# Performance work log

Hardware: AMD Instinct MI355X
Metric: run time of the kernel (lower is better)

## Reference

```python
import jax, jax.numpy as jnp
import numpy as np

N_NODES = 50000
N_EDGES = 800000
D_IN = 128
D_OUT = 128


def setup_inputs() -> dict:
    key = jax.random.key(0)
    k1, k2, k3, k4, k5, k6 = jax.random.split(key, 6)
    x = jax.random.normal(k1, (N_NODES, D_IN), dtype=jnp.float32)
    weight = jax.random.normal(k2, (D_IN, D_OUT), dtype=jnp.float32)
    bias = jax.random.normal(k3, (D_OUT,), dtype=jnp.float32)
    adj_row = jax.random.randint(k4, (N_EDGES,), 0, N_NODES, dtype=jnp.int64)
    adj_col = jax.random.randint(k5, (N_EDGES,), 0, N_NODES, dtype=jnp.int64)
    adj_val = jax.random.uniform(k6, (N_EDGES,), dtype=jnp.float32)
    return {"x": x, "weight": weight, "bias": bias,
            "adj_row": adj_row, "adj_col": adj_col, "adj_val": adj_val}


def reference(x, weight, bias, adj_row, adj_col, adj_val):
    # support = x @ W  -- dense GEMM [N, D_in] x [D_in, D_out]
    support = jnp.matmul(x, weight)
    # spmm(adj, support): out[i] = sum_e adj_val[e] * support[adj_col[e]] for adj_row[e]==i
    messages = support[adj_col] * adj_val[:, None]          # [E, D_out]
    output = jax.ops.segment_sum(messages, adj_row, num_segments=x.shape[0])
    return output + bias
```

## Files before the change

kernel.cpp:

```cpp
#include <hip/hip_runtime.h>

#define D 128
#define ELL_CAP 64
#define EPT 8

typedef __attribute__((ext_vector_type(8))) short short8;
typedef __attribute__((ext_vector_type(4))) float floatx4;
typedef unsigned int uint;
typedef unsigned short ushort;

__device__ inline short f2bf(float f) {
  unsigned u = __float_as_uint(f);
  u += 0x7FFF + ((u >> 16) & 1);
  return (short)(u >> 16);
}

__global__ __launch_bounds__(256) void gemm_scatter_kernel(
    const float* __restrict__ x, const float* __restrict__ w,
    ushort* __restrict__ support, int n_nodes, int gemm_blocks,
    const int* __restrict__ adj_row, const int* __restrict__ adj_col,
    const float* __restrict__ adj_val, int* __restrict__ cnt,
    uint* __restrict__ ell, int n_edges, int range_size) {
  __shared__ short sWA[2 * 8 * 64 * 8];
  const int tid = threadIdx.x;

  if ((int)blockIdx.x < gemm_blocks) {
    const int wid = tid >> 6;
    const int lane = tid & 63;
    const int quad = lane >> 4;
    const int node = blockIdx.x * 64 + wid * 16 + (lane & 15);
    const bool ok = (node < n_nodes);

    floatx4 acc[8];
#pragma unroll
    for (int mt = 0; mt < 8; ++mt) acc[mt] = (floatx4){0.f, 0.f, 0.f, 0.f};

#pragma unroll
    for (int kt2 = 0; kt2 < 4; kt2 += 2) {
      if (kt2) __syncthreads();
      for (int s = tid; s < 1024; s += 256) {
        int ktmt = s >> 6, ls = s & 63;
        int kt = kt2 + (ktmt >> 3);
        int kb = kt * 32 + (ls >> 4) * 8;
        int m = (ktmt & 7) * 16 + (ls & 15);
        short8 frag;
#pragma unroll
        for (int j = 0; j < 8; ++j) frag[j] = f2bf(w[(kb + j) * D + m]);
        *(short8*)&sWA[s * 8] = frag;
      }
      __syncthreads();

#pragma unroll
      for (int ktoff = 0; ktoff < 2; ++ktoff) {
        const int kt = kt2 + ktoff;
        short8 bfr = (short8){0, 0, 0, 0, 0, 0, 0, 0};
        if (ok) {
          const float4 v0 = *(const float4*)&x[(size_t)node * D + kt * 32 + quad * 8];
          const float4 v1 = *(const float4*)&x[(size_t)node * D + kt * 32 + quad * 8 + 4];
          bfr = (short8){f2bf(v0.x), f2bf(v0.y), f2bf(v0.z), f2bf(v0.w),
                         f2bf(v1.x), f2bf(v1.y), f2bf(v1.z), f2bf(v1.w)};
        }
#pragma unroll
        for (int mt = 0; mt < 8; ++mt) {
          short8 a = *(const short8*)&sWA[((ktoff * 8 + mt) * 64 + lane) * 8];
          acc[mt] = __builtin_amdgcn_mfma_f32_16x16x32_bf16(a, bfr, acc[mt], 0, 0, 0);
        }
      }
    }

    if (ok) {
#pragma unroll
      for (int mt = 0; mt < 8; ++mt) {
        uint lo = ((uint)(ushort)f2bf(acc[mt][1]) << 16) | (ushort)f2bf(acc[mt][0]);
        uint hi = ((uint)(ushort)f2bf(acc[mt][3]) << 16) | (ushort)f2bf(acc[mt][2]);
        *(uint2*)&support[(size_t)node * D + mt * 16 + quad * 4] = make_uint2(lo, hi);
      }
    }
  } else {
    const int b = blockIdx.x - gemm_blocks;
    const int g = b & 7;
    const int c = b >> 3;
    const int lo = g * range_size, hi = lo + range_size;
    const int base = c * (256 * EPT) + tid * EPT;

    if (base + EPT <= n_edges) {
      int4 r0 = *(const int4*)&adj_row[base];
      int4 r1 = *(const int4*)&adj_row[base + 4];
      int4 c0 = *(const int4*)&adj_col[base];
      int4 c1 = *(const int4*)&adj_col[base + 4];
      float4 v0 = *(const float4*)&adj_val[base];
      float4 v1 = *(const float4*)&adj_val[base + 4];
      int rr[EPT] = {r0.x, r0.y, r0.z, r0.w, r1.x, r1.y, r1.z, r1.w};
      int cc[EPT] = {c0.x, c0.y, c0.z, c0.w, c1.x, c1.y, c1.z, c1.w};
      float vv[EPT] = {v0.x, v0.y, v0.z, v0.w, v1.x, v1.y, v1.z, v1.w};
#pragma unroll
      for (int u = 0; u < EPT; ++u) {
        int r = rr[u];
        if (r >= lo && r < hi) {
          int pos = atomicAdd(&cnt[r], 1);
          if (pos < ELL_CAP)
            ell[(size_t)r * ELL_CAP + pos] = ((uint)cc[u] << 16) | (ushort)f2bf(vv[u]);
        }
      }
    } else {
      for (int u = 0; u < EPT; ++u) {
        int e = base + u;
        if (e >= n_edges) break;
        int r = adj_row[e];
        if (r >= lo && r < hi) {
          int pos = atomicAdd(&cnt[r], 1);
          if (pos < ELL_CAP)
            ell[(size_t)r * ELL_CAP + pos] = ((uint)adj_col[e] << 16) | (ushort)f2bf(adj_val[e]);
        }
      }
    }
  }
}

__global__ __launch_bounds__(256) void spmm_ell_kernel(const int* __restrict__ cnt,
                                                       const uint* __restrict__ ell,
                                                       const uint* __restrict__ sup,
                                                       const float* __restrict__ bias,
                                                       float* __restrict__ out,
                                                       int n_rows) {
  const int wave = (int)((blockIdx.x * 256 + threadIdx.x) >> 6);
  const int lane = threadIdx.x & 63;
  const int half = lane >> 5;
  const int hl = lane & 31;
  const int r = wave * 2 + half;
  if (wave * 2 >= n_rows) return;

  int n = 0;
  if (r < n_rows) n = cnt[r];
  if (n > ELL_CAP) n = ELL_CAP;
  uint ent0 = 0, ent1 = 0;
  if (hl < n) ent0 = ell[(size_t)r * ELL_CAP + hl];
  if (hl + 32 < n) ent1 = ell[(size_t)r * ELL_CAP + 32 + hl];

  int nmax = n;
  int no = __shfl_xor(nmax, 32);
  if (no > nmax) nmax = no;
  const int m = (nmax + 7) & ~7;

  float a0 = 0.f, a1 = 0.f, a2 = 0.f, a3 = 0.f;
  for (int j = 0; j < m; j += 8) {
    uint e[8];
    uint2 s[8];
#pragma unroll
    for (int u = 0; u < 8; ++u) {
      int jj = j + u;
      int src = (half << 5) + (jj & 31);
      e[u] = __shfl(jj < 32 ? ent0 : ent1, src);
    }
#pragma unroll
    for (int u = 0; u < 8; ++u)
      s[u] = *(const uint2*)&sup[(size_t)(e[u] >> 16) * 64 + hl * 2];
#pragma unroll
    for (int u = 0; u < 8; ++u) {
      float wv = __uint_as_float(e[u] << 16);
      a0 = fmaf(wv, __uint_as_float(s[u].x << 16), a0);
      a1 = fmaf(wv, __uint_as_float(s[u].x & 0xffff0000u), a1);
      a2 = fmaf(wv, __uint_as_float(s[u].y << 16), a2);
      a3 = fmaf(wv, __uint_as_float(s[u].y & 0xffff0000u), a3);
    }
  }

  if (r < n_rows) {
    float4 b = *(const float4*)&bias[hl * 4];
    *(float4*)&out[(size_t)r * D + hl * 4] =
        make_float4(b.x + a0, b.y + a1, b.z + a2, b.w + a3);
  }
}

extern "C" void kernel_launch(void* const* d_in, const int* in_sizes, int n_in,
                              void* d_out, int out_size, void* d_ws, size_t ws_size,
                              hipStream_t stream) {
  const float* x       = (const float*)d_in[0];
  const float* w       = (const float*)d_in[1];
  const float* bias    = (const float*)d_in[2];
  const int*   adj_row = (const int*)d_in[3];
  const int*   adj_col = (const int*)d_in[4];
  const float* adj_val = (const float*)d_in[5];

  const int n_nodes = in_sizes[0] / D;
  const int n_edges = in_sizes[3];
  float* out = (float*)d_out;

  char* ws = (char*)d_ws;
  ushort* support = (ushort*)ws; ws += ((size_t)n_nodes * D * 2 + 15) & ~15ull;
  int*    row_cnt = (int*)ws;    ws += ((size_t)n_nodes * 4 + 15) & ~15ull;
  uint*   ell     = (uint*)ws;   ws += (size_t)n_nodes * ELL_CAP * 4;

  hipMemsetAsync(row_cnt, 0, (size_t)n_nodes * 4, stream);

  const int gemm_blocks = (n_nodes + 63) / 64;
  const int range_size = (n_nodes + 7) / 8;
  const int chunks = (n_edges + 256 * EPT - 1) / (256 * EPT);
  gemm_scatter_kernel<<<gemm_blocks + chunks * 8, 256, 0, stream>>>(
      x, w, support, n_nodes, gemm_blocks,
      adj_row, adj_col, adj_val, row_cnt, ell, n_edges, range_size);

  int waves = (n_nodes + 1) / 2;
  int spmm_blocks = (waves + 3) / 4;
  spmm_ell_kernel<<<spmm_blocks, 256, 0, stream>>>(row_cnt, ell, (const uint*)support,
                                                   bias, out, n_nodes);
}
```

Before: 155.5 us.

## Split support into column-slice planes and gather per-slice in SpMM

```diff
diff --git a/kernel.cpp b/kernel.cpp
--- a/kernel.cpp
+++ b/kernel.cpp
@@ -73,7 +73,9 @@
       for (int mt = 0; mt < 8; ++mt) {
         uint lo = ((uint)(ushort)f2bf(acc[mt][1]) << 16) | (ushort)f2bf(acc[mt][0]);
         uint hi = ((uint)(ushort)f2bf(acc[mt][3]) << 16) | (ushort)f2bf(acc[mt][2]);
-        *(uint2*)&support[(size_t)node * D + mt * 16 + quad * 4] = make_uint2(lo, hi);
+        size_t off = (size_t)(mt >> 1) * n_nodes * 32 +
+                     (size_t)node * 32 + (mt & 1) * 16 + quad * 4;
+        *(uint2*)&support[off] = make_uint2(lo, hi);
       }
     }
   } else {
@@ -123,52 +125,64 @@
                                                        const float* __restrict__ bias,
                                                        float* __restrict__ out,
                                                        int n_rows) {
-  const int wave = (int)((blockIdx.x * 256 + threadIdx.x) >> 6);
-  const int lane = threadIdx.x & 63;
-  const int half = lane >> 5;
-  const int hl = lane & 31;
-  const int r = wave * 2 + half;
-  if (wave * 2 >= n_rows) return;
+  const int slice = blockIdx.x & 3;
+  const int chunk = blockIdx.x >> 2;
+  const int tid = threadIdx.x;
+  const int wid = tid >> 6;
+  const int lane = tid & 63;
+  const int team = lane >> 2;
+  const int sub = lane & 3;
+  const int r = chunk * 64 + wid * 16 + team;
+  const uint* plane = sup + (size_t)slice * n_rows * 16;
 
   int n = 0;
   if (r < n_rows) n = cnt[r];
   if (n > ELL_CAP) n = ELL_CAP;
-  uint ent0 = 0, ent1 = 0;
-  if (hl < n) ent0 = ell[(size_t)r * ELL_CAP + hl];
-  if (hl + 32 < n) ent1 = ell[(size_t)r * ELL_CAP + 32 + hl];
-
-  int nmax = n;
-  int no = __shfl_xor(nmax, 32);
-  if (no > nmax) nmax = no;
-  const int m = (nmax + 7) & ~7;
+
+  int nmax = n, t;
+  t = __shfl_xor(nmax, 4);  if (t > nmax) nmax = t;
+  t = __shfl_xor(nmax, 8);  if (t > nmax) nmax = t;
+  t = __shfl_xor(nmax, 16); if (t > nmax) nmax = t;
+  t = __shfl_xor(nmax, 32); if (t > nmax) nmax = t;
 
   float a0 = 0.f, a1 = 0.f, a2 = 0.f, a3 = 0.f;
-  for (int j = 0; j < m; j += 8) {
-    uint e[8];
-    uint2 s[8];
-#pragma unroll
-    for (int u = 0; u < 8; ++u) {
-      int jj = j + u;
-      int src = (half << 5) + (jj & 31);
-      e[u] = __shfl(jj < 32 ? ent0 : ent1, src);
-    }
-#pragma unroll
-    for (int u = 0; u < 8; ++u)
-      s[u] = *(const uint2*)&sup[(size_t)(e[u] >> 16) * 64 + hl * 2];
-#pragma unroll
-    for (int u = 0; u < 8; ++u) {
-      float wv = __uint_as_float(e[u] << 16);
-      a0 = fmaf(wv, __uint_as_float(s[u].x << 16), a0);
-      a1 = fmaf(wv, __uint_as_float(s[u].x & 0xffff0000u), a1);
-      a2 = fmaf(wv, __uint_as_float(s[u].y << 16), a2);
-      a3 = fmaf(wv, __uint_as_float(s[u].y & 0xffff0000u), a3);
+  float a4 = 0.f, a5 = 0.f, a6 = 0.f, a7 = 0.f;
+  const int tbase = lane & 0x3c;
+
+  for (int seg = 0; seg < 4; ++seg) {
+    const int j0 = seg * 16;
+    if (j0 >= nmax) break;
+    uint4 lent = make_uint4(0, 0, 0, 0);
+    if (r < n_rows && j0 < n)
+      lent = *(const uint4*)&ell[(size_t)r * ELL_CAP + j0 + sub * 4];
+#pragma unroll
+    for (int u = 0; u < 16; ++u) {
+      if (j0 + u < n) {
+        uint comp = (u & 3) == 0 ? lent.x : (u & 3) == 1 ? lent.y
+                  : (u & 3) == 2 ? lent.z : lent.w;
+        uint e = __shfl(comp, tbase + (u >> 2));
+        uint4 s4 = *(const uint4*)&plane[(size_t)(e >> 16) * 16 + sub * 4];
+        float wv = __uint_as_float(e << 16);
+        a0 = fmaf(wv, __uint_as_float(s4.x << 16), a0);
+        a1 = fmaf(wv, __uint_as_float(s4.x & 0xffff0000u), a1);
+        a2 = fmaf(wv, __uint_as_float(s4.y << 16), a2);
+        a3 = fmaf(wv, __uint_as_float(s4.y & 0xffff0000u), a3);
+        a4 = fmaf(wv, __uint_as_float(s4.z << 16), a4);
+        a5 = fmaf(wv, __uint_as_float(s4.z & 0xffff0000u), a5);
+        a6 = fmaf(wv, __uint_as_float(s4.w << 16), a6);
+        a7 = fmaf(wv, __uint_as_float(s4.w & 0xffff0000u), a7);
+      }
     }
   }
 
   if (r < n_rows) {
-    float4 b = *(const float4*)&bias[hl * 4];
-    *(float4*)&out[(size_t)r * D + hl * 4] =
-        make_float4(b.x + a0, b.y + a1, b.z + a2, b.w + a3);
+    const int f0 = slice * 32 + sub * 8;
+    float4 b0 = *(const float4*)&bias[f0];
+    float4 b1 = *(const float4*)&bias[f0 + 4];
+    *(float4*)&out[(size_t)r * D + f0] =
+        make_float4(b0.x + a0, b0.y + a1, b0.z + a2, b0.w + a3);
+    *(float4*)&out[(size_t)r * D + f0 + 4] =
+        make_float4(b1.x + a4, b1.y + a5, b1.z + a6, b1.w + a7);
   }
 }
 
@@ -200,8 +214,8 @@
       x, w, support, n_nodes, gemm_blocks,
       adj_row, adj_col, adj_val, row_cnt, ell, n_edges, range_size);
 
-  int waves = (n_nodes + 1) / 2;
-  int spmm_blocks = (waves + 3) / 4;
-  spmm_ell_kernel<<<spmm_blocks, 256, 0, stream>>>(row_cnt, ell, (const uint*)support,
-                                                   bias, out, n_nodes);
-}
+  const int row_chunks = (n_nodes + 63) / 64;
+  spmm_ell_kernel<<<row_chunks * 4, 256, 0, stream>>>(row_cnt, ell,
+                                                      (const uint*)support,
+                                                      bias, out, n_nodes);
+}
```

After: 161.0 us. 3.5% more time.
